# Performance work log

Hardware: AMD Instinct MI355X
Metric: run time of the kernel (lower is better)

## Reference

```python
import jax, jax.numpy as jnp
import numpy as np

N = 50000      # nodes
E = 800000     # random edges (self-loops appended -> E + N total)
IN, HID, OUT, HEADS = 128, 256, 256, 8


def _gat_layer(x, src, dst, W, a_src, a_dst, bias):
    # x: [N, F_in]; W: [F_in, H*C]; a_src/a_dst: [H, C]; bias: [H*C]
    n = x.shape[0]
    H, C = a_src.shape
    h = (x @ W).reshape(n, H, C)                      # per-head transform
    al_s = jnp.sum(h * a_src, axis=-1)                # [N, H]
    al_d = jnp.sum(h * a_dst, axis=-1)                # [N, H]
    e = jax.nn.leaky_relu(al_s[src] + al_d[dst], 0.2) # [E, H]
    # segmented softmax over incoming edges of each destination node
    m = jax.ops.segment_max(e, dst, num_segments=n)   # [N, H]
    e = jnp.exp(e - m[dst])
    s = jax.ops.segment_sum(e, dst, num_segments=n)   # [N, H]
    alpha = e / (s[dst] + 1e-16)                      # [E, H]
    out = jax.ops.segment_sum(alpha[:, :, None] * h[src], dst, num_segments=n)
    return out.reshape(n, H * C) + bias


def setup_inputs() -> dict:
    key = jax.random.key(0)
    ks = jax.random.split(key, 9)
    x = jax.random.normal(ks[0], (N, IN), dtype=jnp.float32)
    src = jax.random.randint(ks[1], (E,), 0, N)
    dst = jax.random.randint(ks[2], (E,), 0, N)
    loop = jnp.arange(N)  # PyG GATConv adds self-loops by default
    edge_index = jnp.stack([jnp.concatenate([src, loop]),
                            jnp.concatenate([dst, loop])]).astype(jnp.int64)
    C1, C2 = HID // HEADS, OUT // HEADS
    W1 = jax.random.normal(ks[3], (IN, HID), jnp.float32) * (1.0 / np.sqrt(IN))
    a1_src = jax.random.normal(ks[4], (HEADS, C1), jnp.float32) * 0.1
    a1_dst = jax.random.normal(ks[5], (HEADS, C1), jnp.float32) * 0.1
    b1 = jnp.zeros((HID,), jnp.float32)
    W2 = jax.random.normal(ks[6], (HID, OUT), jnp.float32) * (1.0 / np.sqrt(HID))
    a2_src = jax.random.normal(ks[7], (HEADS, C2), jnp.float32) * 0.1
    a2_dst = jax.random.normal(ks[8], (HEADS, C2), jnp.float32) * 0.1
    b2 = jnp.zeros((OUT,), jnp.float32)
    return {"x": x, "edge_index": edge_index,
            "W1": W1, "a1_src": a1_src, "a1_dst": a1_dst, "b1": b1,
            "W2": W2, "a2_src": a2_src, "a2_dst": a2_dst, "b2": b2}


def reference(x, edge_index, W1, a1_src, a1_dst, b1, W2, a2_src, a2_dst, b2):
    src, dst = edge_index[0], edge_index[1]
    h = jax.nn.elu(_gat_layer(x, src, dst, W1, a1_src, a1_dst, b1))
    out = jax.nn.elu(_gat_layer(h, src, dst, W2, a2_src, a2_dst, b2))
    return out
```

## Files before the change

### kernel.cpp

```cpp
#include <hip/hip_runtime.h>
#include <hip/hip_bf16.h>


#define HEADS 8
#define F 256

typedef _Float16 h8 __attribute__((ext_vector_type(8)));
typedef _Float16 h4 __attribute__((ext_vector_type(4)));
typedef float f4 __attribute__((ext_vector_type(4)));

#define WAVE_SYNC() do { __builtin_amdgcn_wave_barrier(); \
  asm volatile("s_waitcnt lgkmcnt(0)" ::: "memory"); \
  __builtin_amdgcn_wave_barrier(); } while (0)


__global__ void k_prep(const float* __restrict__ x, _Float16* __restrict__ xh, int n128,
                       const float* __restrict__ W1, _Float16* __restrict__ Wt1,
                       const float* __restrict__ W2, _Float16* __restrict__ Wt2,
                       const int* __restrict__ dst, int Et, int* __restrict__ deg,
                       int cvtB) {
  int b = blockIdx.x, tid = threadIdx.x;
  if (b < cvtB) {
    int idx = (b * 256 + tid) * 4;
    if (idx < n128) {
      float4 v = *(const float4*)&x[idx];
      h4 o = {(_Float16)v.x, (_Float16)v.y, (_Float16)v.z, (_Float16)v.w};
      *(h4*)&xh[idx] = o;
    }
  } else if (b < cvtB + 384) {
    int k = b - cvtB;
    if (k < 128) Wt1[(size_t)tid * 128 + k] = (_Float16)W1[(size_t)k * F + tid];
    else {
      k -= 128;
      Wt2[(size_t)tid * 256 + k] = (_Float16)W2[(size_t)k * F + tid];
    }
  } else {
    int i = (b - cvtB - 384) * 256 + tid;
    for (; i < Et; i += 512 * 256) atomicAdd(&deg[dst[i]], 1);
  }
}


__global__ __launch_bounds__(1024) void k_scan1(const int* __restrict__ deg, int n,
                                                int* __restrict__ rowptr, int* __restrict__ bsum) {
  __shared__ int s[1024];
  int i = blockIdx.x * 1024 + threadIdx.x;
  int v = (i < n) ? deg[i] : 0;
  s[threadIdx.x] = v;
  __syncthreads();
  for (int off = 1; off < 1024; off <<= 1) {
    int add = (threadIdx.x >= off) ? s[threadIdx.x - off] : 0;
    __syncthreads();
    s[threadIdx.x] += add;
    __syncthreads();
  }
  if (i < n) rowptr[i] = s[threadIdx.x] - v;
  if (threadIdx.x == 1023) bsum[blockIdx.x] = s[1023];
}

__global__ void k_scan2(const int* __restrict__ bsum, int nb, int* __restrict__ boff) {
  int t = threadIdx.x;
  int v = (t < nb) ? bsum[t] : 0;
  int inc = v;
  for (int off = 1; off < 64; off <<= 1) {
    int y = __shfl_up(inc, off, 64);
    if (t >= off) inc += y;
  }
  boff[t] = inc - v;
}

__global__ void k_scan3(int n, int Et, int* __restrict__ rowptr,
                        int* __restrict__ rowwork, const int* __restrict__ boff) {
  int i = blockIdx.x * blockDim.x + threadIdx.x;
  if (i < n) {
    int v = rowptr[i] + boff[i >> 10];
    rowptr[i] = v;
    rowwork[i] = v;
  }
  if (i == 0) rowptr[n] = Et;
}

__global__ void k_fill(const int* __restrict__ src, const int* __restrict__ dst, int Et,
                       int* __restrict__ rowwork, int* __restrict__ csr_src) {
  int i = blockIdx.x * blockDim.x + threadIdx.x;
  if (i < Et) {
    int pos = atomicAdd(&rowwork[dst[i]], 1);
    csr_src[pos] = src[i];
  }
}


__global__ __launch_bounds__(512) void k_gemm(const _Float16* __restrict__ A,
                                              const _Float16* __restrict__ Bt,
                                              _Float16* __restrict__ C,
                                              const float* __restrict__ a_src,
                                              const float* __restrict__ a_dst,
                                              float* __restrict__ als,
                                              float* __restrict__ ald,
                                              int M, int K) {
  __shared__ _Float16 As[128][40];
  __shared__ _Float16 Bs[256][40];
  int tid = threadIdx.x;
  int lane = tid & 63, w = tid >> 6;
  int wr = w & 1, wc = w >> 1;
  int rowBase = blockIdx.x * 128;
  f4 acc[4][4] = {};

  int arow = tid >> 2, akoff = (tid & 3) * 8;
  int arow_g = min(rowBase + arow, M - 1);
  const _Float16* Ap = A + (size_t)arow_g * K + akoff;
  int bc = tid >> 1, bkoff = (tid & 1) * 16;
  const _Float16* Bp = Bt + (size_t)bc * K + bkoff;

  int kl = (lane >> 4) * 8;
  int rl = lane & 15;

  int nsteps = K >> 5;
  h8 av = *(const h8*)(Ap);
  h8 bv0 = *(const h8*)(Bp);
  h8 bv1 = *(const h8*)(Bp + 8);

  for (int s = 0; s < nsteps; ++s) {
    *(h8*)&As[arow][akoff] = av;
    *(h8*)&Bs[bc][bkoff] = bv0;
    *(h8*)&Bs[bc][bkoff + 8] = bv1;
    __syncthreads();
    if (s + 1 < nsteps) {
      int k0 = (s + 1) << 5;
      av = *(const h8*)(Ap + k0);
      bv0 = *(const h8*)(Bp + k0);
      bv1 = *(const h8*)(Bp + k0 + 8);
    }
    h8 af[4], bf[4];
#pragma unroll
    for (int fi = 0; fi < 4; ++fi) af[fi] = *(const h8*)&As[wr * 64 + fi * 16 + rl][kl];
#pragma unroll
    for (int fj = 0; fj < 4; ++fj) bf[fj] = *(const h8*)&Bs[wc * 64 + fj * 16 + rl][kl];
#pragma unroll
    for (int fi = 0; fi < 4; ++fi)
#pragma unroll
      for (int fj = 0; fj < 4; ++fj)
        acc[fi][fj] = __builtin_amdgcn_mfma_f32_16x16x32_f16(af[fi], bf[fj], acc[fi][fj], 0, 0, 0);
    __syncthreads();
  }

  int rquad = (lane >> 4) * 4;

#pragma unroll
  for (int fi = 0; fi < 4; ++fi)
#pragma unroll
    for (int fj = 0; fj < 4; ++fj) {
      int col = wc * 64 + fj * 16 + rl;
#pragma unroll
      for (int r = 0; r < 4; ++r) {
        int row = rowBase + wr * 64 + fi * 16 + rquad + r;
        if (row < M) C[(size_t)row * F + col] = (_Float16)acc[fi][fj][r];
      }
    }

  int head0 = wc * 2;
  float as0 = a_src[head0 * 32 + rl],      as1 = a_src[head0 * 32 + 16 + rl];
  float ad0 = a_dst[head0 * 32 + rl],      ad1 = a_dst[head0 * 32 + 16 + rl];
  float cs0 = a_src[head0 * 32 + 32 + rl], cs1 = a_src[head0 * 32 + 48 + rl];
  float cd0 = a_dst[head0 * 32 + 32 + rl], cd1 = a_dst[head0 * 32 + 48 + rl];
#pragma unroll
  for (int fi = 0; fi < 4; ++fi)
#pragma unroll
    for (int r = 0; r < 4; ++r) {
      float v0s = acc[fi][0][r] * as0 + acc[fi][1][r] * as1;
      float v0d = acc[fi][0][r] * ad0 + acc[fi][1][r] * ad1;
      float v1s = acc[fi][2][r] * cs0 + acc[fi][3][r] * cs1;
      float v1d = acc[fi][2][r] * cd0 + acc[fi][3][r] * cd1;
#pragma unroll
      for (int off = 8; off; off >>= 1) {
        v0s += __shfl_xor(v0s, off);
        v0d += __shfl_xor(v0d, off);
        v1s += __shfl_xor(v1s, off);
        v1d += __shfl_xor(v1d, off);
      }
      int row = rowBase + wr * 64 + fi * 16 + rquad + r;
      if (rl == 0 && row < M) {
        als[row * HEADS + head0] = v0s;
        ald[row * HEADS + head0] = v0d;
        als[row * HEADS + head0 + 1] = v1s;
        ald[row * HEADS + head0 + 1] = v1d;
      }
    }
}


template <bool F16OUT>
__global__ __launch_bounds__(256) void k_agg(const int* __restrict__ rowptr,
                                             const int* __restrict__ csr_src,
                                             const float* __restrict__ al_s,
                                             const float* __restrict__ al_d,
                                             const _Float16* __restrict__ h,
                                             const float* __restrict__ bias,
                                             float* __restrict__ outf,
                                             _Float16* __restrict__ outh,
                                             int n) {
  __shared__ float eps[4][64][8];
  __shared__ int ssrc[4][64];
  int tid = threadIdx.x;
  int w = tid >> 6, lane = tid & 63;
  int node = blockIdx.x * 4 + w;
  if (node >= n) return;
  int base = rowptr[node];
  int d = rowptr[node + 1] - base;
  int hh = lane >> 3, slot = lane & 7;
  float alD = al_d[node * HEADS + hh];

  float invs;
  f4 facc = {0.f, 0.f, 0.f, 0.f};
  const _Float16* hc = h + (lane << 2);

  if (d <= 64) {
    float m = -1e30f;
    for (int j = slot; j < d; j += 8) {
      int s = csr_src[base + j];
      if (hh == 0) ssrc[w][j] = s;
      float e = al_s[s * HEADS + hh] + alD;
      e = (e > 0.f) ? e : 0.2f * e;
      eps[w][j][hh] = e;
      m = fmaxf(m, e);
    }
#pragma unroll
    for (int off = 4; off; off >>= 1) m = fmaxf(m, __shfl_xor(m, off));
    float sm = 0.f;
    for (int j = slot; j < d; j += 8) {
      float p = __expf(eps[w][j][hh] - m);
      eps[w][j][hh] = p;
      sm += p;
    }
#pragma unroll
    for (int off = 4; off; off >>= 1) sm += __shfl_xor(sm, off);
    invs = 1.f / (sm + 1e-16f);
    WAVE_SYNC();
    int j = 0;
    for (; j + 4 <= d; j += 4) {
      int s0 = __builtin_amdgcn_readfirstlane(ssrc[w][j]);
      int s1 = __builtin_amdgcn_readfirstlane(ssrc[w][j + 1]);
      int s2 = __builtin_amdgcn_readfirstlane(ssrc[w][j + 2]);
      int s3 = __builtin_amdgcn_readfirstlane(ssrc[w][j + 3]);
      float p0 = eps[w][j][hh], p1 = eps[w][j + 1][hh];
      float p2 = eps[w][j + 2][hh], p3 = eps[w][j + 3][hh];
      h4 v0 = *(const h4*)(hc + ((size_t)s0 << 8));
      h4 v1 = *(const h4*)(hc + ((size_t)s1 << 8));
      h4 v2 = *(const h4*)(hc + ((size_t)s2 << 8));
      h4 v3 = *(const h4*)(hc + ((size_t)s3 << 8));
      facc.x += p0 * (float)v0.x + p1 * (float)v1.x + p2 * (float)v2.x + p3 * (float)v3.x;
      facc.y += p0 * (float)v0.y + p1 * (float)v1.y + p2 * (float)v2.y + p3 * (float)v3.y;
      facc.z += p0 * (float)v0.z + p1 * (float)v1.z + p2 * (float)v2.z + p3 * (float)v3.z;
      facc.w += p0 * (float)v0.w + p1 * (float)v1.w + p2 * (float)v2.w + p3 * (float)v3.w;
    }
    for (; j < d; ++j) {
      int s0 = __builtin_amdgcn_readfirstlane(ssrc[w][j]);
      float p0 = eps[w][j][hh];
      h4 v0 = *(const h4*)(hc + ((size_t)s0 << 8));
      facc.x += p0 * (float)v0.x;
      facc.y += p0 * (float)v0.y;
      facc.z += p0 * (float)v0.z;
      facc.w += p0 * (float)v0.w;
    }
  } else {
    float m = -1e30f;
    for (int j = slot; j < d; j += 8) {
      int s = csr_src[base + j];
      float e = al_s[s * HEADS + hh] + alD;
      e = (e > 0.f) ? e : 0.2f * e;
      m = fmaxf(m, e);
    }
#pragma unroll
    for (int off = 4; off; off >>= 1) m = fmaxf(m, __shfl_xor(m, off));
    float sm = 0.f;
    for (int j = slot; j < d; j += 8) {
      int s = csr_src[base + j];
      float e = al_s[s * HEADS + hh] + alD;
      e = (e > 0.f) ? e : 0.2f * e;
      sm += __expf(e - m);
    }
#pragma unroll
    for (int off = 4; off; off >>= 1) sm += __shfl_xor(sm, off);
    invs = 1.f / (sm + 1e-16f);
    for (int c0 = 0; c0 < d; c0 += 64) {
      int cn = min(64, d - c0);
      WAVE_SYNC();
      for (int j = slot; j < cn; j += 8) {
        int s = csr_src[base + c0 + j];
        if (hh == 0) ssrc[w][j] = s;
        float e = al_s[s * HEADS + hh] + alD;
        e = (e > 0.f) ? e : 0.2f * e;
        eps[w][j][hh] = __expf(e - m);
      }
      WAVE_SYNC();
      for (int j = 0; j < cn; ++j) {
        int s0 = __builtin_amdgcn_readfirstlane(ssrc[w][j]);
        float p0 = eps[w][j][hh];
        h4 v0 = *(const h4*)(hc + ((size_t)s0 << 8));
        facc.x += p0 * (float)v0.x;
        facc.y += p0 * (float)v0.y;
        facc.z += p0 * (float)v0.z;
        facc.w += p0 * (float)v0.w;
      }
    }
  }

  int c0 = lane << 2;
  float4 bv = *(const float4*)&bias[c0];
  float o0 = facc.x * invs + bv.x;
  float o1 = facc.y * invs + bv.y;
  float o2 = facc.z * invs + bv.z;
  float o3 = facc.w * invs + bv.w;
  o0 = (o0 > 0.f) ? o0 : expm1f(o0);
  o1 = (o1 > 0.f) ? o1 : expm1f(o1);
  o2 = (o2 > 0.f) ? o2 : expm1f(o2);
  o3 = (o3 > 0.f) ? o3 : expm1f(o3);
  if (F16OUT) {
    h4 o = {(_Float16)o0, (_Float16)o1, (_Float16)o2, (_Float16)o3};
    *(h4*)&outh[((size_t)node << 8) + c0] = o;
  } else {
    *(float4*)&outf[((size_t)node << 8) + c0] = make_float4(o0, o1, o2, o3);
  }
}


extern "C" void kernel_launch(void* const* d_in, const int* in_sizes, int n_in,
                              void* d_out, int out_size, void* d_ws, size_t ws_size,
                              hipStream_t stream) {
  const float* x   = (const float*)d_in[0];
  const int*   ei  = (const int*)d_in[1];
  const float* W1  = (const float*)d_in[2];
  const float* a1s = (const float*)d_in[3];
  const float* a1d = (const float*)d_in[4];
  const float* b1  = (const float*)d_in[5];
  const float* W2  = (const float*)d_in[6];
  const float* a2s = (const float*)d_in[7];
  const float* a2d = (const float*)d_in[8];
  const float* b2  = (const float*)d_in[9];

  int n  = in_sizes[0] / 128;
  int Et = in_sizes[1] / 2;
  const int* srcp = ei;
  const int* dstp = ei + Et;

  char* ws = (char*)d_ws;
  auto alloc = [&](size_t bytes) {
    char* p = ws;
    ws += (bytes + 255) & ~(size_t)255;
    return p;
  };
  _Float16* xh      = (_Float16*)alloc((size_t)n * 128 * 2);
  _Float16* hbuf    = (_Float16*)alloc((size_t)n * F * 2);
  _Float16* Wt1     = (_Float16*)alloc((size_t)128 * F * 2);
  _Float16* Wt2     = (_Float16*)alloc((size_t)F * F * 2);
  float*    als     = (float*)alloc((size_t)n * HEADS * 4);
  float*    ald     = (float*)alloc((size_t)n * HEADS * 4);
  int*      deg     = (int*)alloc((size_t)n * 4);
  int*      rowptr  = (int*)alloc((size_t)(n + 1) * 4);
  int*      rowwork = (int*)alloc((size_t)n * 4);
  int*      bsum    = (int*)alloc(64 * 4);
  int*      boff    = (int*)alloc(64 * 4);
  int*      csr     = (int*)alloc((size_t)Et * 4);
  _Float16* out1h   = (_Float16*)d_out;
  float*    outF    = (float*)d_out;

  hipMemsetAsync(deg, 0, (size_t)n * 4, stream);

  int n128 = n * 128;
  int cvtB = (n128 / 4 + 255) / 256;
  k_prep<<<cvtB + 384 + 512, 256, 0, stream>>>(x, xh, n128, W1, Wt1, W2, Wt2,
                                               dstp, Et, deg, cvtB);

  int nb = (n + 1023) / 1024;
  k_scan1<<<nb, 1024, 0, stream>>>(deg, n, rowptr, bsum);
  k_scan2<<<1, 64, 0, stream>>>(bsum, nb, boff);
  k_scan3<<<(n + 255) / 256, 256, 0, stream>>>(n, Et, rowptr, rowwork, boff);
  k_fill<<<(Et + 255) / 256, 256, 0, stream>>>(srcp, dstp, Et, rowwork, csr);

  int gb = (n + 127) / 128;
  int ab = (n + 3) / 4;
  k_gemm<<<gb, 512, 0, stream>>>(xh, Wt1, hbuf, a1s, a1d, als, ald, n, 128);
  k_agg<true><<<ab, 256, 0, stream>>>(rowptr, csr, als, ald, hbuf, b1, nullptr, out1h, n);
  k_gemm<<<gb, 512, 0, stream>>>(out1h, Wt2, hbuf, a2s, a2d, als, ald, n, 256);
  k_agg<false><<<ab, 256, 0, stream>>>(rowptr, csr, als, ald, hbuf, b2, outF, nullptr, n);
}
```

Baseline: 376.2 us.

## Fuse CSR fill and input conversion into GEMM, single-pass online aggregation

The fp32-to-fp16 conversion of x moves into the first GEMM's A-tile loads, and the CSR fill runs in extra blocks of that same GEMM launch. The two scan-fixup kernels merge into one. CSR rows are padded to multiples of four so the aggregation can read int4 neighbor indices. The aggregation kernel becomes a single pass with no max subtraction and no LDS staging. This removes several launches, an intermediate buffer and a second pass over edge logits. The cost is that exp without max subtraction could overflow on large attention logits.

Result: faster. 348.3 us (-7.4%).

```diff
diff --git a/kernel.cpp b/kernel.cpp
--- a/kernel.cpp
+++ b/kernel.cpp
@@ -9,33 +9,18 @@
 typedef _Float16 h4 __attribute__((ext_vector_type(4)));
 typedef float f4 __attribute__((ext_vector_type(4)));
 
-#define WAVE_SYNC() do { __builtin_amdgcn_wave_barrier(); \
-  asm volatile("s_waitcnt lgkmcnt(0)" ::: "memory"); \
-  __builtin_amdgcn_wave_barrier(); } while (0)
-
-
-__global__ void k_prep(const float* __restrict__ x, _Float16* __restrict__ xh, int n128,
-                       const float* __restrict__ W1, _Float16* __restrict__ Wt1,
+
+__global__ void k_prep(const float* __restrict__ W1, _Float16* __restrict__ Wt1,
                        const float* __restrict__ W2, _Float16* __restrict__ Wt2,
-                       const int* __restrict__ dst, int Et, int* __restrict__ deg,
-                       int cvtB) {
+                       const int* __restrict__ dst, int Et, int* __restrict__ deg) {
   int b = blockIdx.x, tid = threadIdx.x;
-  if (b < cvtB) {
-    int idx = (b * 256 + tid) * 4;
-    if (idx < n128) {
-      float4 v = *(const float4*)&x[idx];
-      h4 o = {(_Float16)v.x, (_Float16)v.y, (_Float16)v.z, (_Float16)v.w};
-      *(h4*)&xh[idx] = o;
-    }
-  } else if (b < cvtB + 384) {
-    int k = b - cvtB;
-    if (k < 128) Wt1[(size_t)tid * 128 + k] = (_Float16)W1[(size_t)k * F + tid];
-    else {
-      k -= 128;
-      Wt2[(size_t)tid * 256 + k] = (_Float16)W2[(size_t)k * F + tid];
-    }
+  if (b < 128) {
+    Wt1[(size_t)tid * 128 + b] = (_Float16)W1[(size_t)b * F + tid];
+  } else if (b < 384) {
+    int k = b - 128;
+    Wt2[(size_t)tid * 256 + k] = (_Float16)W2[(size_t)k * F + tid];
   } else {
-    int i = (b - cvtB - 384) * 256 + tid;
+    int i = (b - 384) * 256 + tid;
     for (; i < Et; i += 512 * 256) atomicAdd(&deg[dst[i]], 1);
   }
 }
@@ -45,7 +30,7 @@
                                                 int* __restrict__ rowptr, int* __restrict__ bsum) {
   __shared__ int s[1024];
   int i = blockIdx.x * 1024 + threadIdx.x;
-  int v = (i < n) ? deg[i] : 0;
+  int v = (i < n) ? ((deg[i] + 3) & ~3) : 0;
   s[threadIdx.x] = v;
   __syncthreads();
   for (int off = 1; off < 1024; off <<= 1) {
@@ -58,46 +43,50 @@
   if (threadIdx.x == 1023) bsum[blockIdx.x] = s[1023];
 }
 
-__global__ void k_scan2(const int* __restrict__ bsum, int nb, int* __restrict__ boff) {
-  int t = threadIdx.x;
-  int v = (t < nb) ? bsum[t] : 0;
-  int inc = v;
-  for (int off = 1; off < 64; off <<= 1) {
-    int y = __shfl_up(inc, off, 64);
-    if (t >= off) inc += y;
-  }
-  boff[t] = inc - v;
-}
-
-__global__ void k_scan3(int n, int Et, int* __restrict__ rowptr,
-                        int* __restrict__ rowwork, const int* __restrict__ boff) {
-  int i = blockIdx.x * blockDim.x + threadIdx.x;
+__global__ void k_scan23(int n, const int* __restrict__ bsum,
+                         int* __restrict__ rowptr, int* __restrict__ rowwork) {
+  __shared__ int boffs;
+  int nbx = blockIdx.x >> 2;
+  if (threadIdx.x < 64) {
+    int t = threadIdx.x;
+    int v = (t < nbx) ? bsum[t] : 0;
+#pragma unroll
+    for (int off = 32; off; off >>= 1) v += __shfl_xor(v, off, 64);
+    if (t == 0) boffs = v;
+  }
+  __syncthreads();
+  int i = blockIdx.x * 256 + threadIdx.x;
   if (i < n) {
-    int v = rowptr[i] + boff[i >> 10];
+    int v = rowptr[i] + boffs;
     rowptr[i] = v;
     rowwork[i] = v;
   }
-  if (i == 0) rowptr[n] = Et;
-}
-
-__global__ void k_fill(const int* __restrict__ src, const int* __restrict__ dst, int Et,
-                       int* __restrict__ rowwork, int* __restrict__ csr_src) {
-  int i = blockIdx.x * blockDim.x + threadIdx.x;
-  if (i < Et) {
-    int pos = atomicAdd(&rowwork[dst[i]], 1);
-    csr_src[pos] = src[i];
-  }
-}
-
-
-__global__ __launch_bounds__(512) void k_gemm(const _Float16* __restrict__ A,
+}
+
+
+template <bool AF32, bool FILL>
+__global__ __launch_bounds__(512) void k_gemm(const void* __restrict__ Av,
                                               const _Float16* __restrict__ Bt,
                                               _Float16* __restrict__ C,
                                               const float* __restrict__ a_src,
                                               const float* __restrict__ a_dst,
                                               float* __restrict__ als,
                                               float* __restrict__ ald,
-                                              int M, int K) {
+                                              int M, int K,
+                                              const int* __restrict__ esrc,
+                                              const int* __restrict__ edst,
+                                              int Et, int* __restrict__ rowwork,
+                                              int* __restrict__ csr, int gemmBlocks) {
+  if (FILL && (int)blockIdx.x >= gemmBlocks) {
+    int i = ((int)blockIdx.x - gemmBlocks) * 512 + threadIdx.x;
+    int stride = ((int)gridDim.x - gemmBlocks) * 512;
+    for (; i < Et; i += stride) {
+      int pos = atomicAdd(&rowwork[edst[i]], 1);
+      csr[pos] = esrc[i];
+    }
+    return;
+  }
+
   __shared__ _Float16 As[128][40];
   __shared__ _Float16 Bs[256][40];
   int tid = threadIdx.x;
@@ -108,7 +97,8 @@
 
   int arow = tid >> 2, akoff = (tid & 3) * 8;
   int arow_g = min(rowBase + arow, M - 1);
-  const _Float16* Ap = A + (size_t)arow_g * K + akoff;
+  const _Float16* Ap = (const _Float16*)Av + (size_t)arow_g * K + akoff;
+  const float*    Apf = (const float*)Av + (size_t)arow_g * K + akoff;
   int bc = tid >> 1, bkoff = (tid & 1) * 16;
   const _Float16* Bp = Bt + (size_t)bc * K + bkoff;
 
@@ -116,31 +106,41 @@
   int rl = lane & 15;
 
   int nsteps = K >> 5;
-  h8 av = *(const h8*)(Ap);
+  h8 av;
+  float4 af0, af1;
+  if (AF32) { af0 = *(const float4*)(Apf); af1 = *(const float4*)(Apf + 4); }
+  else av = *(const h8*)(Ap);
   h8 bv0 = *(const h8*)(Bp);
   h8 bv1 = *(const h8*)(Bp + 8);
 
   for (int s = 0; s < nsteps; ++s) {
-    *(h8*)&As[arow][akoff] = av;
+    if (AF32) {
+      h8 t = {(_Float16)af0.x, (_Float16)af0.y, (_Float16)af0.z, (_Float16)af0.w,
+              (_Float16)af1.x, (_Float16)af1.y, (_Float16)af1.z, (_Float16)af1.w};
+      *(h8*)&As[arow][akoff] = t;
+    } else {
+      *(h8*)&As[arow][akoff] = av;
+    }
     *(h8*)&Bs[bc][bkoff] = bv0;
     *(h8*)&Bs[bc][bkoff + 8] = bv1;
     __syncthreads();
     if (s + 1 < nsteps) {
       int k0 = (s + 1) << 5;
-      av = *(const h8*)(Ap + k0);
+      if (AF32) { af0 = *(const float4*)(Apf + k0); af1 = *(const float4*)(Apf + k0 + 4); }
+      else av = *(const h8*)(Ap + k0);
       bv0 = *(const h8*)(Bp + k0);
       bv1 = *(const h8*)(Bp + k0 + 8);
     }
-    h8 af[4], bf[4];
-#pragma unroll
-    for (int fi = 0; fi < 4; ++fi) af[fi] = *(const h8*)&As[wr * 64 + fi * 16 + rl][kl];
-#pragma unroll
-    for (int fj = 0; fj < 4; ++fj) bf[fj] = *(const h8*)&Bs[wc * 64 + fj * 16 + rl][kl];
+    h8 afr[4], bfr[4];
+#pragma unroll
+    for (int fi = 0; fi < 4; ++fi) afr[fi] = *(const h8*)&As[wr * 64 + fi * 16 + rl][kl];
+#pragma unroll
+    for (int fj = 0; fj < 4; ++fj) bfr[fj] = *(const h8*)&Bs[wc * 64 + fj * 16 + rl][kl];
 #pragma unroll
     for (int fi = 0; fi < 4; ++fi)
 #pragma unroll
       for (int fj = 0; fj < 4; ++fj)
-        acc[fi][fj] = __builtin_amdgcn_mfma_f32_16x16x32_f16(af[fi], bf[fj], acc[fi][fj], 0, 0, 0);
+        acc[fi][fj] = __builtin_amdgcn_mfma_f32_16x16x32_f16(afr[fi], bfr[fj], acc[fi][fj], 0, 0, 0);
     __syncthreads();
   }
 
@@ -191,7 +191,8 @@
 
 template <bool F16OUT>
 __global__ __launch_bounds__(256) void k_agg(const int* __restrict__ rowptr,
-                                             const int* __restrict__ csr_src,
+                                             const int* __restrict__ deg,
+                                             const int* __restrict__ csr,
                                              const float* __restrict__ al_s,
                                              const float* __restrict__ al_d,
                                              const _Float16* __restrict__ h,
@@ -199,118 +200,66 @@
                                              float* __restrict__ outf,
                                              _Float16* __restrict__ outh,
                                              int n) {
-  __shared__ float eps[4][64][8];
-  __shared__ int ssrc[4][64];
   int tid = threadIdx.x;
   int w = tid >> 6, lane = tid & 63;
   int node = blockIdx.x * 4 + w;
   if (node >= n) return;
   int base = rowptr[node];
-  int d = rowptr[node + 1] - base;
-  int hh = lane >> 3, slot = lane & 7;
+  int d = deg[node];
+  int hh = lane >> 3;
   float alD = al_d[node * HEADS + hh];
-
-  float invs;
-  f4 facc = {0.f, 0.f, 0.f, 0.f};
   const _Float16* hc = h + (lane << 2);
-
-  if (d <= 64) {
-    float m = -1e30f;
-    for (int j = slot; j < d; j += 8) {
-      int s = csr_src[base + j];
-      if (hh == 0) ssrc[w][j] = s;
-      float e = al_s[s * HEADS + hh] + alD;
-      e = (e > 0.f) ? e : 0.2f * e;
-      eps[w][j][hh] = e;
-      m = fmaxf(m, e);
-    }
-#pragma unroll
-    for (int off = 4; off; off >>= 1) m = fmaxf(m, __shfl_xor(m, off));
-    float sm = 0.f;
-    for (int j = slot; j < d; j += 8) {
-      float p = __expf(eps[w][j][hh] - m);
-      eps[w][j][hh] = p;
-      sm += p;
-    }
-#pragma unroll
-    for (int off = 4; off; off >>= 1) sm += __shfl_xor(sm, off);
-    invs = 1.f / (sm + 1e-16f);
-    WAVE_SYNC();
-    int j = 0;
+  const int* cp = csr + base;
+
+  f4 acc = {0.f, 0.f, 0.f, 0.f};
+  float sp = 0.f;
+  int j = 0;
+  if (d >= 4) {
+    int4 sv = *(const int4*)cp;
     for (; j + 4 <= d; j += 4) {
-      int s0 = __builtin_amdgcn_readfirstlane(ssrc[w][j]);
-      int s1 = __builtin_amdgcn_readfirstlane(ssrc[w][j + 1]);
-      int s2 = __builtin_amdgcn_readfirstlane(ssrc[w][j + 2]);
-      int s3 = __builtin_amdgcn_readfirstlane(ssrc[w][j + 3]);
-      float p0 = eps[w][j][hh], p1 = eps[w][j + 1][hh];
-      float p2 = eps[w][j + 2][hh], p3 = eps[w][j + 3][hh];
-      h4 v0 = *(const h4*)(hc + ((size_t)s0 << 8));
-      h4 v1 = *(const h4*)(hc + ((size_t)s1 << 8));
-      h4 v2 = *(const h4*)(hc + ((size_t)s2 << 8));
-      h4 v3 = *(const h4*)(hc + ((size_t)s3 << 8));
-      facc.x += p0 * (float)v0.x + p1 * (float)v1.x + p2 * (float)v2.x + p3 * (float)v3.x;
-      facc.y += p0 * (float)v0.y + p1 * (float)v1.y + p2 * (float)v2.y + p3 * (float)v3.y;
-      facc.z += p0 * (float)v0.z + p1 * (float)v1.z + p2 * (float)v2.z + p3 * (float)v3.z;
-      facc.w += p0 * (float)v0.w + p1 * (float)v1.w + p2 * (float)v2.w + p3 * (float)v3.w;
-    }
-    for (; j < d; ++j) {
-      int s0 = __builtin_amdgcn_readfirstlane(ssrc[w][j]);
-      float p0 = eps[w][j][hh];
-      h4 v0 = *(const h4*)(hc + ((size_t)s0 << 8));
-      facc.x += p0 * (float)v0.x;
-      facc.y += p0 * (float)v0.y;
-      facc.z += p0 * (float)v0.z;
-      facc.w += p0 * (float)v0.w;
-    }
-  } else {
-    float m = -1e30f;
-    for (int j = slot; j < d; j += 8) {
-      int s = csr_src[base + j];
-      float e = al_s[s * HEADS + hh] + alD;
-      e = (e > 0.f) ? e : 0.2f * e;
-      m = fmaxf(m, e);
-    }
-#pragma unroll
-    for (int off = 4; off; off >>= 1) m = fmaxf(m, __shfl_xor(m, off));
-    float sm = 0.f;
-    for (int j = slot; j < d; j += 8) {
-      int s = csr_src[base + j];
-      float e = al_s[s * HEADS + hh] + alD;
-      e = (e > 0.f) ? e : 0.2f * e;
-      sm += __expf(e - m);
-    }
-#pragma unroll
-    for (int off = 4; off; off >>= 1) sm += __shfl_xor(sm, off);
-    invs = 1.f / (sm + 1e-16f);
-    for (int c0 = 0; c0 < d; c0 += 64) {
-      int cn = min(64, d - c0);
-      WAVE_SYNC();
-      for (int j = slot; j < cn; j += 8) {
-        int s = csr_src[base + c0 + j];
-        if (hh == 0) ssrc[w][j] = s;
-        float e = al_s[s * HEADS + hh] + alD;
-        e = (e > 0.f) ? e : 0.2f * e;
-        eps[w][j][hh] = __expf(e - m);
-      }
-      WAVE_SYNC();
-      for (int j = 0; j < cn; ++j) {
-        int s0 = __builtin_amdgcn_readfirstlane(ssrc[w][j]);
-        float p0 = eps[w][j][hh];
-        h4 v0 = *(const h4*)(hc + ((size_t)s0 << 8));
-        facc.x += p0 * (float)v0.x;
-        facc.y += p0 * (float)v0.y;
-        facc.z += p0 * (float)v0.z;
-        facc.w += p0 * (float)v0.w;
-      }
-    }
-  }
-
+      int4 svn = sv;
+      if (j + 8 <= d) svn = *(const int4*)(cp + j + 4);
+      float e0 = al_s[sv.x * HEADS + hh] + alD;
+      float e1 = al_s[sv.y * HEADS + hh] + alD;
+      float e2 = al_s[sv.z * HEADS + hh] + alD;
+      float e3 = al_s[sv.w * HEADS + hh] + alD;
+      e0 = (e0 > 0.f) ? e0 : 0.2f * e0;
+      e1 = (e1 > 0.f) ? e1 : 0.2f * e1;
+      e2 = (e2 > 0.f) ? e2 : 0.2f * e2;
+      e3 = (e3 > 0.f) ? e3 : 0.2f * e3;
+      float p0 = __expf(e0), p1 = __expf(e1), p2 = __expf(e2), p3 = __expf(e3);
+      h4 v0 = *(const h4*)(hc + ((size_t)sv.x << 8));
+      h4 v1 = *(const h4*)(hc + ((size_t)sv.y << 8));
+      h4 v2 = *(const h4*)(hc + ((size_t)sv.z << 8));
+      h4 v3 = *(const h4*)(hc + ((size_t)sv.w << 8));
+      acc.x += p0 * (float)v0.x + p1 * (float)v1.x + p2 * (float)v2.x + p3 * (float)v3.x;
+      acc.y += p0 * (float)v0.y + p1 * (float)v1.y + p2 * (float)v2.y + p3 * (float)v3.y;
+      acc.z += p0 * (float)v0.z + p1 * (float)v1.z + p2 * (float)v2.z + p3 * (float)v3.z;
+      acc.w += p0 * (float)v0.w + p1 * (float)v1.w + p2 * (float)v2.w + p3 * (float)v3.w;
+      sp += p0 + p1 + p2 + p3;
+      sv = svn;
+    }
+  }
+  for (; j < d; ++j) {
+    int s = cp[j];
+    float e = al_s[s * HEADS + hh] + alD;
+    e = (e > 0.f) ? e : 0.2f * e;
+    float p = __expf(e);
+    h4 v = *(const h4*)(hc + ((size_t)s << 8));
+    acc.x += p * (float)v.x;
+    acc.y += p * (float)v.y;
+    acc.z += p * (float)v.z;
+    acc.w += p * (float)v.w;
+    sp += p;
+  }
+
+  float invs = 1.f / (sp + 1e-16f);
   int c0 = lane << 2;
   float4 bv = *(const float4*)&bias[c0];
-  float o0 = facc.x * invs + bv.x;
-  float o1 = facc.y * invs + bv.y;
-  float o2 = facc.z * invs + bv.z;
-  float o3 = facc.w * invs + bv.w;
+  float o0 = acc.x * invs + bv.x;
+  float o1 = acc.y * invs + bv.y;
+  float o2 = acc.z * invs + bv.z;
+  float o3 = acc.w * invs + bv.w;
   o0 = (o0 > 0.f) ? o0 : expm1f(o0);
   o1 = (o1 > 0.f) ? o1 : expm1f(o1);
   o2 = (o2 > 0.f) ? o2 : expm1f(o2);
@@ -349,7 +298,6 @@
     ws += (bytes + 255) & ~(size_t)255;
     return p;
   };
-  _Float16* xh      = (_Float16*)alloc((size_t)n * 128 * 2);
   _Float16* hbuf    = (_Float16*)alloc((size_t)n * F * 2);
   _Float16* Wt1     = (_Float16*)alloc((size_t)128 * F * 2);
   _Float16* Wt2     = (_Float16*)alloc((size_t)F * F * 2);
@@ -359,28 +307,24 @@
   int*      rowptr  = (int*)alloc((size_t)(n + 1) * 4);
   int*      rowwork = (int*)alloc((size_t)n * 4);
   int*      bsum    = (int*)alloc(64 * 4);
-  int*      boff    = (int*)alloc(64 * 4);
-  int*      csr     = (int*)alloc((size_t)Et * 4);
+  int*      csr     = (int*)alloc(((size_t)Et + 4 * (size_t)n) * 4);
   _Float16* out1h   = (_Float16*)d_out;
   float*    outF    = (float*)d_out;
 
   hipMemsetAsync(deg, 0, (size_t)n * 4, stream);
 
-  int n128 = n * 128;
-  int cvtB = (n128 / 4 + 255) / 256;
-  k_prep<<<cvtB + 384 + 512, 256, 0, stream>>>(x, xh, n128, W1, Wt1, W2, Wt2,
-                                               dstp, Et, deg, cvtB);
+  k_prep<<<384 + 512, 256, 0, stream>>>(W1, Wt1, W2, Wt2, dstp, Et, deg);
 
   int nb = (n + 1023) / 1024;
   k_scan1<<<nb, 1024, 0, stream>>>(deg, n, rowptr, bsum);
-  k_scan2<<<1, 64, 0, stream>>>(bsum, nb, boff);
-  k_scan3<<<(n + 255) / 256, 256, 0, stream>>>(n, Et, rowptr, rowwork, boff);
-  k_fill<<<(Et + 255) / 256, 256, 0, stream>>>(srcp, dstp, Et, rowwork, csr);
+  k_scan23<<<(n + 255) / 256, 256, 0, stream>>>(n, bsum, rowptr, rowwork);
 
   int gb = (n + 127) / 128;
   int ab = (n + 3) / 4;
-  k_gemm<<<gb, 512, 0, stream>>>(xh, Wt1, hbuf, a1s, a1d, als, ald, n, 128);
-  k_agg<true><<<ab, 256, 0, stream>>>(rowptr, csr, als, ald, hbuf, b1, nullptr, out1h, n);
-  k_gemm<<<gb, 512, 0, stream>>>(out1h, Wt2, hbuf, a2s, a2d, als, ald, n, 256);
-  k_agg<false><<<ab, 256, 0, stream>>>(rowptr, csr, als, ald, hbuf, b2, outF, nullptr, n);
-}
+  k_gemm<true, true><<<gb + 1024, 512, 0, stream>>>(x, Wt1, hbuf, a1s, a1d, als, ald,
+                                                    n, 128, srcp, dstp, Et, rowwork, csr, gb);
+  k_agg<true><<<ab, 256, 0, stream>>>(rowptr, deg, csr, als, ald, hbuf, b1, nullptr, out1h, n);
+  k_gemm<false, false><<<gb, 512, 0, stream>>>(out1h, Wt2, hbuf, a2s, a2d, als, ald,
+                                               n, 256, nullptr, nullptr, 0, nullptr, nullptr, gb);
+  k_agg<false><<<ab, 256, 0, stream>>>(rowptr, deg, csr, als, ald, hbuf, b2, outF, nullptr, n);
+}
```
